# Optimization experiments

Hardware: AMD Instinct MI355X
Metric: run time of the kernel (lower is better)

Reference implementation:

```python
import jax, jax.numpy as jnp
import numpy as np

# ---- config (mirrors init_kwargs) ----
D_MODEL = 1024
D_STATE = 128
EXPAND = 2
HEADDIM = 64
D_INNER = D_MODEL * EXPAND            # 2048
NHEADS = D_INNER // HEADDIM           # 32
ROPE_FRACTION = 0.5
ROTATE_DIM = (int(D_STATE * ROPE_FRACTION) // 2) * 2   # 64
NUM_ANGLES = ROTATE_DIM // 2          # 32
A_FLOOR = 1e-4
EPS = 1e-5
IN_PROJ_DIM = 2 * D_INNER + 2 * D_STATE + 3 * NHEADS + NUM_ANGLES  # 4480
BATCH, SEQLEN = 2, 2048


def _state_rmsnorm(x, w):
    rms = jnp.sqrt(jnp.mean(x * x, axis=-1, keepdims=True) + EPS)
    return x / rms * w


def _apply_rotary_pairs(x, phase):
    # x: (b,s,h,d_state), phase: (b,s,h,num_pairs)
    if ROTATE_DIM == 0:
        return x
    x_rot = x[..., :ROTATE_DIM].reshape(*x.shape[:-1], ROTATE_DIM // 2, 2)
    x_pass = x[..., ROTATE_DIM:]
    cos = jnp.cos(phase)
    sin = jnp.sin(phase)
    real = x_rot[..., 0]
    imag = x_rot[..., 1]
    rr = real * cos - imag * sin
    ri = real * sin + imag * cos
    rotated = jnp.stack([rr, ri], axis=-1).reshape(*x.shape[:-1], ROTATE_DIM)
    if x_pass.shape[-1] == 0:
        return rotated
    return jnp.concatenate([rotated, x_pass], axis=-1)


def setup_inputs() -> dict:
    key = jax.random.key(0)
    ks = jax.random.split(key, 5)
    x = jax.random.normal(ks[0], (BATCH, SEQLEN, D_MODEL), jnp.float32)
    W_in = jax.random.normal(ks[1], (IN_PROJ_DIM, D_MODEL), jnp.float32) / np.sqrt(D_MODEL)
    # dt_bias ~ inverse-softplus of dt sampled in [dt_min, dt_max]
    dt = jnp.exp(jax.random.uniform(ks[2], (NHEADS,), jnp.float32) * (np.log(0.1) - np.log(0.001)) + np.log(0.001))
    dt = jnp.clip(dt, 1e-4)
    dt_bias = dt + jnp.log(-jnp.expm1(-dt))
    B_norm_w = jnp.ones((D_STATE,), jnp.float32)
    C_norm_w = jnp.ones((D_STATE,), jnp.float32)
    B_bias = jnp.ones((NHEADS, D_STATE), jnp.float32)
    C_bias = jnp.ones((NHEADS, D_STATE), jnp.float32)
    D_param = jnp.ones((NHEADS,), jnp.float32)
    out_norm_w = jnp.ones((D_INNER,), jnp.float32)
    W_out = jax.random.normal(ks[3], (D_MODEL, D_INNER), jnp.float32) / np.sqrt(D_INNER)
    return {"x": x, "W_in": W_in, "dt_bias": dt_bias, "B_norm_w": B_norm_w,
            "C_norm_w": C_norm_w, "B_bias": B_bias, "C_bias": C_bias,
            "D_param": D_param, "out_norm_w": out_norm_w, "W_out": W_out}


def reference(x, W_in, dt_bias, B_norm_w, C_norm_w, B_bias, C_bias, D_param, out_norm_w, W_out):
    b, s, _ = x.shape
    proj = jnp.einsum('bsd,pd->bsp', x, W_in)
    sizes = [D_INNER, D_INNER, D_STATE, D_STATE, NHEADS, NHEADS, NHEADS, NUM_ANGLES]
    offs = np.cumsum([0] + sizes)
    z, v, B_raw, C_raw, dd_dt, dd_A, trap_logits, angle_logits = [
        proj[..., offs[i]:offs[i + 1]] for i in range(8)]
    z = z.reshape(b, s, NHEADS, HEADDIM)
    v = v.reshape(b, s, NHEADS, HEADDIM)
    Bm = _state_rmsnorm(B_raw, B_norm_w)[:, :, None, :] + B_bias[None, None]   # (b,s,h,n)
    Cm = _state_rmsnorm(C_raw, C_norm_w)[:, :, None, :] + C_bias[None, None]
    dt = jax.nn.softplus(dd_dt + dt_bias[None, None])          # (b,s,h)
    A = jnp.minimum(-jax.nn.softplus(dd_A), -A_FLOOR)          # (b,s,h)
    trap = jax.nn.sigmoid(trap_logits)                          # (b,s,h)
    phase = jnp.cumsum(angle_logits, axis=1)[:, :, None, :]     # (b,s,1,angles)
    phase = jnp.broadcast_to(phase, (b, s, NHEADS, NUM_ANGLES))
    Bm = _apply_rotary_pairs(Bm, phase)
    Cm = _apply_rotary_pairs(Cm, phase)

    alpha = jnp.exp(A * dt)               # (b,s,h)
    beta = (1.0 - trap) * dt * alpha
    gamma = trap * dt

    # move time to leading for scan: (s, b, h, ...)
    def tl(a):
        return jnp.moveaxis(a, 1, 0)
    xs = (tl(alpha), tl(beta), tl(gamma), tl(Bm), tl(Cm), tl(v))

    state0 = jnp.zeros((b, NHEADS, HEADDIM, D_STATE), jnp.float32)
    pk0 = jnp.zeros((b, NHEADS, D_STATE), jnp.float32)
    pv0 = jnp.zeros((b, NHEADS, HEADDIM), jnp.float32)

    def step(carry, inp):
        state, pk, pv = carry
        a_t, b_t, g_t, k_t, q_t, v_t = inp
        prev_outer = pv[..., :, None] * pk[..., None, :]        # (b,h,p,n)
        curr_outer = v_t[..., :, None] * k_t[..., None, :]
        state = (a_t[..., None, None] * state
                 + b_t[..., None, None] * prev_outer
                 + g_t[..., None, None] * curr_outer)
        y_t = jnp.einsum('bhpn,bhn->bhp', state, q_t) + D_param[None, :, None] * v_t
        return (state, k_t, v_t), y_t

    _, ys = jax.lax.scan(step, (state0, pk0, pv0), xs)
    y = jnp.moveaxis(ys, 0, 1).reshape(b, s, D_INNER)
    z = z.reshape(b, s, D_INNER)
    # GatedRMSNorm
    rms = jnp.sqrt(jnp.mean(y * y, axis=-1, keepdims=True) + EPS)
    y = (y / rms * out_norm_w) * jax.nn.silu(z)
    return jnp.einsum('bsi,di->bsd', y, W_out)
```

## Files before the change

### kernel.cpp

```cpp
#include <hip/hip_runtime.h>
#include <math.h>

#define S_LEN 2048
#define NBATCH 2
#define DMODEL 1024
#define PDIM 4480
#define DI 2048
#define NH 32
#define HD 64
#define DS 128
#define NA 32
#define CHK 64
#define NC (S_LEN / CHK)
#define OFF_Z 0
#define OFF_V 2048
#define OFF_B 4096
#define OFF_C 4224
#define OFF_DT 4352
#define OFF_A 4384
#define OFF_TRAP 4416
#define OFF_ANG 4448

typedef __attribute__((ext_vector_type(8))) short s8v;
typedef __attribute__((ext_vector_type(4))) float f4v;

__device__ __forceinline__ float softplus_f(float x) {
    return x > 20.f ? x : log1pf(expf(x));
}

__device__ __forceinline__ ushort f2bf(float f) {
    unsigned u = __float_as_uint(f);
    unsigned r = (u + 0x7fffu + ((u >> 16) & 1u)) >> 16;
    return (ushort)r;
}

__device__ __forceinline__ uint4 pack8(const float* f) {
    uint4 o;
    o.x = (unsigned)f2bf(f[0]) | ((unsigned)f2bf(f[1]) << 16);
    o.y = (unsigned)f2bf(f[2]) | ((unsigned)f2bf(f[3]) << 16);
    o.z = (unsigned)f2bf(f[4]) | ((unsigned)f2bf(f[5]) << 16);
    o.w = (unsigned)f2bf(f[6]) | ((unsigned)f2bf(f[7]) << 16);
    return o;
}

__device__ __forceinline__ float bf2f(ushort u) {
    return __uint_as_float(((unsigned)u) << 16);
}
__device__ __forceinline__ float bf_lo(unsigned u) { return __uint_as_float(u << 16); }
__device__ __forceinline__ float bf_hi(unsigned u) { return __uint_as_float(u & 0xffff0000u); }

#define NCX  524288
#define NCWI 573440
#define NCWO 262144
__global__ __launch_bounds__(256)
void f2bf_all(const float* __restrict__ x, const float* __restrict__ wi,
              const float* __restrict__ wo, ushort* __restrict__ xbf,
              ushort* __restrict__ wibf, ushort* __restrict__ wobf) {
    int idx = blockIdx.x * 256 + threadIdx.x;
    const float* src; ushort* dst; int shift, rel;
    if (idx < NCX)              { rel = idx;               src = x;  dst = xbf;  shift = 7; }
    else if (idx < NCX + NCWI)  { rel = idx - NCX;         src = wi; dst = wibf; shift = 7; }
    else                        { rel = idx - NCX - NCWI;  src = wo; dst = wobf; shift = 8; }
    int dc = rel ^ ((rel >> shift) & 7);
    const float* ip = src + (size_t)rel * 8;
    float4 v0 = *(const float4*)ip;
    float4 v1 = *(const float4*)(ip + 4);
    uint4 o;
    o.x = (unsigned)f2bf(v0.x) | ((unsigned)f2bf(v0.y) << 16);
    o.y = (unsigned)f2bf(v0.z) | ((unsigned)f2bf(v0.w) << 16);
    o.z = (unsigned)f2bf(v1.x) | ((unsigned)f2bf(v1.y) << 16);
    o.w = (unsigned)f2bf(v1.z) | ((unsigned)f2bf(v1.w) << 16);
    *(uint4*)(dst + (size_t)dc * 8) = o;
}

__global__ __launch_bounds__(256, 4)
void gemm_bf16(const ushort* __restrict__ A, const ushort* __restrict__ B,
               float* __restrict__ C, int M, int N, int K) {
    __shared__ __align__(16) short lA[128 * 64];
    __shared__ __align__(16) short lB[128 * 64];
    int nwg = gridDim.x;
    int bid = blockIdx.x;
    int q = nwg >> 3;
    int swz = (bid & 7) * q + (bid >> 3);
    int nb = N >> 7;
    int bx = swz % nb, by = swz / nb;

    int tid = threadIdx.x;
    int wv = tid >> 6, ln = tid & 63;
    int rl = ln & 15, kg = ln >> 4, r7 = rl & 7;
    int R0 = (wv >> 1) * 64, C0 = (wv & 1) * 64;

    const ushort* Ag = A + (size_t)(by * 128 + wv * 32 + (ln >> 3)) * K + (ln & 7) * 8;
    const ushort* Bg = B + (size_t)(bx * 128 + wv * 32 + (ln >> 3)) * K + (ln & 7) * 8;
    short* lAw = lA + (wv * 32) * 64;
    short* lBw = lB + (wv * 32) * 64;

    f4v acc[4][4];
#pragma unroll
    for (int m = 0; m < 4; ++m)
#pragma unroll
        for (int n = 0; n < 4; ++n) acc[m][n] = f4v{0.f, 0.f, 0.f, 0.f};

    for (int k0 = 0; k0 < K; k0 += 64) {
        __syncthreads();
#pragma unroll
        for (int i = 0; i < 4; ++i) {
            __builtin_amdgcn_global_load_lds(
                (const __attribute__((address_space(1))) void*)(Ag + (size_t)i * 8 * K + k0),
                (__attribute__((address_space(3))) void*)(lAw + i * 8 * 64), 16, 0, 0);
            __builtin_amdgcn_global_load_lds(
                (const __attribute__((address_space(1))) void*)(Bg + (size_t)i * 8 * K + k0),
                (__attribute__((address_space(3))) void*)(lBw + i * 8 * 64), 16, 0, 0);
        }
        __syncthreads();
#pragma unroll
        for (int ks = 0; ks < 2; ++ks) {
            int kc = ks * 4 + kg;
            int co = ((kc ^ r7) << 3);
            s8v av[4], bv[4];
#pragma unroll
            for (int m = 0; m < 4; ++m)
                av[m] = *(const s8v*)&lA[(R0 + m * 16 + rl) * 64 + co];
#pragma unroll
            for (int n = 0; n < 4; ++n)
                bv[n] = *(const s8v*)&lB[(C0 + n * 16 + rl) * 64 + co];
#pragma unroll
            for (int m = 0; m < 4; ++m)
#pragma unroll
                for (int n = 0; n < 4; ++n)
                    acc[m][n] = __builtin_amdgcn_mfma_f32_16x16x32_bf16(
                        av[m], bv[n], acc[m][n], 0, 0, 0);
        }
    }
#pragma unroll
    for (int m = 0; m < 4; ++m)
#pragma unroll
        for (int n = 0; n < 4; ++n) {
            size_t row0 = (size_t)(by * 128 + R0 + m * 16 + kg * 4);
            int col = bx * 128 + C0 + n * 16 + rl;
#pragma unroll
            for (int r = 0; r < 4; ++r)
                C[(row0 + r) * N + col] = acc[m][n][r];
        }
}

__global__ __launch_bounds__(256)
void phase_kernel(const float* __restrict__ proj, float* __restrict__ cosb,
                  float* __restrict__ sinb) {
    int b = blockIdx.x >> 5;
    int j = blockIdx.x & 31;
    int tid = threadIdx.x;
    __shared__ float part[256];
    float v[8];
    float run = 0.f;
#pragma unroll
    for (int e = 0; e < 8; ++e) {
        int s = tid * 8 + e;
        v[e] = proj[((size_t)(b * S_LEN + s)) * PDIM + OFF_ANG + j];
        run += v[e];
    }
    part[tid] = run;
    __syncthreads();
    for (int off = 1; off < 256; off <<= 1) {
        float add = (tid >= off) ? part[tid - off] : 0.f;
        __syncthreads();
        part[tid] += add;
        __syncthreads();
    }
    float acc = (tid > 0) ? part[tid - 1] : 0.f;
#pragma unroll
    for (int e = 0; e < 8; ++e) {
        acc += v[e];
        int s = tid * 8 + e;
        size_t o = ((size_t)(b * S_LEN + s)) * NA + j;
        cosb[o] = cosf(acc);
        sinb[o] = sinf(acc);
    }
}

__global__ __launch_bounds__(128)
void prep_kernel(const float* __restrict__ proj, const float* __restrict__ dt_bias,
                 const float* __restrict__ Bw, const float* __restrict__ Cw,
                 const float* __restrict__ cosb, const float* __restrict__ sinb,
                 float* __restrict__ Bn, float* __restrict__ Cn,
                 float* __restrict__ ldb, float* __restrict__ wbuf,
                 float* __restrict__ pubuf) {
    size_t row = blockIdx.x;
    int b = (int)(row >> 11);
    int s = (int)(row & 2047);
    int n = threadIdx.x;
    const float* pr = proj + row * PDIM;
    float vB = pr[OFF_B + n];
    float vC = pr[OFF_C + n];
    float sB = vB * vB, sC = vC * vC;
#pragma unroll
    for (int off = 32; off >= 1; off >>= 1) {
        sB += __shfl_xor(sB, off);
        sC += __shfl_xor(sC, off);
    }
    __shared__ float redB[2], redC[2];
    if ((n & 63) == 0) { redB[n >> 6] = sB; redC[n >> 6] = sC; }
    __syncthreads();
    float rB = sqrtf((redB[0] + redB[1]) * (1.f / 128.f) + 1e-5f);
    float rC = sqrtf((redC[0] + redC[1]) * (1.f / 128.f) + 1e-5f);
    float bn = vB / rB * Bw[n];
    float cn = vC / rC * Cw[n];
    float bp = __shfl_xor(bn, 1);
    float cp = __shfl_xor(cn, 1);
    float ob = bn, oc = cn;
    if (n < 64) {
        float c = cosb[row * NA + (n >> 1)];
        float sn_ = sinb[row * NA + (n >> 1)];
        if ((n & 1) == 0) { ob = bn * c - bp * sn_; oc = cn * c - cp * sn_; }
        else              { ob = bp * sn_ + bn * c; oc = cp * sn_ + cn * c; }
    }
    Bn[row * DS + n] = ob;
    Cn[row * DS + n] = oc;
    if (n < NH) {
        int h = n;
        float dtv = softplus_f(pr[OFF_DT + h] + dt_bias[h]);
        float Av = -fmaxf(softplus_f(pr[OFF_A + h]), 1e-4f);
        float trap = 1.f / (1.f + expf(-pr[OFF_TRAP + h]));
        size_t o = ((size_t)(b * NH + h)) * S_LEN + s;
        ldb[o]   = Av * dtv;
        wbuf[o]  = trap * dtv;
        pubuf[o] = (1.f - trap) * dtv;
    }
}

__global__ __launch_bounds__(256)
void lcum_kernel(float* __restrict__ ell) {
    size_t row = blockIdx.x;
    int tid = threadIdx.x;
    float* p = ell + row * S_LEN;
    float v[8];
    float run = 0.f;
#pragma unroll
    for (int e = 0; e < 8; ++e) { v[e] = p[tid * 8 + e]; run += v[e]; }
    __shared__ float part[256];
    part[tid] = run;
    __syncthreads();
    for (int off = 1; off < 256; off <<= 1) {
        float add = (tid >= off) ? part[tid - off] : 0.f;
        __syncthreads();
        part[tid] += add;
        __syncthreads();
    }
    float acc = (tid > 0) ? part[tid - 1] : 0.f;
#pragma unroll
    for (int e = 0; e < 8; ++e) { acc += v[e]; p[tid * 8 + e] = acc; }
}

__device__ __forceinline__ void build32v(
    float* vals, const float* __restrict__ br, const float* __restrict__ bias,
    const float* __restrict__ cr, const float* __restrict__ sr, int rot) {
    float bv[32], bi[32];
#pragma unroll
    for (int j = 0; j < 8; ++j) *(float4*)&bv[j * 4] = *(const float4*)(br + j * 4);
#pragma unroll
    for (int j = 0; j < 8; ++j) *(float4*)&bi[j * 4] = *(const float4*)(bias + j * 4);
    if (rot) {
        float cf[16], sf[16];
#pragma unroll
        for (int j = 0; j < 4; ++j) {
            *(float4*)&cf[j * 4] = *(const float4*)(cr + j * 4);
            *(float4*)&sf[j * 4] = *(const float4*)(sr + j * 4);
        }
#pragma unroll
        for (int a = 0; a < 16; ++a) {
            float c = cf[a], s = sf[a], e = bi[2 * a], o = bi[2 * a + 1];
            vals[2 * a]     = bv[2 * a]     + e * c - o * s;
            vals[2 * a + 1] = bv[2 * a + 1] + e * s + o * c;
        }
    } else {
#pragma unroll
        for (int j = 0; j < 32; ++j) vals[j] = bv[j] + bi[j];
    }
}

__global__ __launch_bounds__(256, 4)
void delta_kernel(const float* __restrict__ proj, const float* __restrict__ Bn,
                  const float* __restrict__ cosb, const float* __restrict__ sinb,
                  const float* __restrict__ ell, const float* __restrict__ wbuf,
                  const float* __restrict__ pubuf, const float* __restrict__ B_bias,
                  ushort* __restrict__ dstate, ushort* __restrict__ vtbuf,
                  float* __restrict__ rbuf) {
    __shared__ __align__(16) ushort KT[DS * CHK];
    __shared__ __align__(16) ushort cVT[HD * CHK];
    __shared__ __align__(16) ushort VT[HD * CHK];
    int blk = blockIdx.x;
    int c = blk & (NC - 1);
    int h = (blk >> 5) & (NH - 1);
    int b = blk >> 10;
    int tid = threadIdx.x;
    size_t row0 = (size_t)b * S_LEN + c * CHK;
    size_t bh = (size_t)b * NH + h;
    int i = tid >> 2, q4 = tid & 3;

    size_t so = bh * S_LEN + c * CHK + i;
    float llast = ell[bh * S_LEN + c * CHK + CHK - 1];
    float li = ell[so];
    float u = wbuf[so];
    if (c * CHK + i < S_LEN - 1) u += pubuf[so + 1];
    float coef = expf(llast - li) * u;
    if (tid == 0) {
        float base = (c == 0) ? 0.f : ell[bh * S_LEN + c * CHK - 1];
        rbuf[blk] = expf(llast - base);
    }
    {
        int n0 = q4 * 32;
        float vals[32];
        build32v(vals, Bn + (row0 + i) * DS + n0, B_bias + h * DS + n0,
                 cosb + (row0 + i) * NA + q4 * 16, sinb + (row0 + i) * NA + q4 * 16,
                 q4 < 2);
#pragma unroll
        for (int j = 0; j < 32; ++j) {
            int n = n0 + j;
            KT[n * 64 + (((i >> 3) ^ (n & 7)) << 3) + (i & 7)] = f2bf(vals[j]);
        }
    }
    {
        int p0 = q4 * 16;
        float vr[16];
        const float* vp = proj + (row0 + i) * PDIM + OFF_V + h * HD + p0;
#pragma unroll
        for (int j = 0; j < 4; ++j) *(float4*)&vr[j * 4] = *(const float4*)(vp + j * 4);
#pragma unroll
        for (int j = 0; j < 16; ++j) {
            int p = p0 + j;
            int addr = p * 64 + (((i >> 3) ^ (p & 7)) << 3) + (i & 7);
            VT[addr]  = f2bf(vr[j]);
            cVT[addr] = f2bf(vr[j] * coef);
        }
    }
    __syncthreads();
    {
        const uint4* vs = (const uint4*)VT;
        uint4* vd = (uint4*)(vtbuf + (size_t)blk * (HD * CHK));
        vd[tid] = vs[tid];
        vd[tid + 256] = vs[tid + 256];
    }
    int wv = tid >> 6, ln = tid & 63, rl = ln & 15, kg = ln >> 4;
    int pA = wv * 16 + rl;
    s8v aV[2];
#pragma unroll
    for (int ks = 0; ks < 2; ++ks)
        aV[ks] = *(const s8v*)&cVT[pA * 64 + (((ks * 4 + kg) ^ (pA & 7)) << 3)];
    ushort* dp = dstate + (size_t)blk * (HD * DS);
#pragma unroll
    for (int nt = 0; nt < 8; ++nt) {
        int nB = nt * 16 + rl;
        f4v dacc = f4v{0.f, 0.f, 0.f, 0.f};
#pragma unroll
        for (int ks = 0; ks < 2; ++ks) {
            s8v bK = *(const s8v*)&KT[nB * 64 + (((ks * 4 + kg) ^ (nB & 7)) << 3)];
            dacc = __builtin_amdgcn_mfma_f32_16x16x32_bf16(aV[ks], bK, dacc, 0, 0, 0);
        }
#pragma unroll
        for (int r = 0; r < 4; ++r) {
            int p = wv * 16 + kg * 4 + r;
            int n = nt * 16 + rl;
            dp[p * DS + (((n >> 3) ^ (p & 7)) << 3) + (n & 7)] = f2bf(dacc[r]);
        }
    }
}

__global__ __launch_bounds__(256)
void state_prop(ushort* __restrict__ dstate, const float* __restrict__ rbuf) {
    size_t bh = blockIdx.x;
    int tid = threadIdx.x;
    float st[32];
#pragma unroll
    for (int j = 0; j < 32; ++j) st[j] = 0.f;
    uint4* base = (uint4*)dstate;
    size_t b0 = bh * NC * 1024ull;
    uint4 nxt[4];
#pragma unroll
    for (int j = 0; j < 4; ++j) nxt[j] = base[b0 + tid * 4 + j];
    for (int c = 0; c < NC; ++c) {
        uint4 cur[4];
#pragma unroll
        for (int j = 0; j < 4; ++j) cur[j] = nxt[j];
        if (c + 1 < NC) {
#pragma unroll
            for (int j = 0; j < 4; ++j)
                nxt[j] = base[b0 + (size_t)(c + 1) * 1024 + tid * 4 + j];
        }
        float r = rbuf[bh * NC + c];
        uint4 outv[4];
#pragma unroll
        for (int j = 0; j < 4; ++j) {
            unsigned uu[4] = {cur[j].x, cur[j].y, cur[j].z, cur[j].w};
            unsigned oo[4];
#pragma unroll
            for (int e = 0; e < 4; ++e) {
                float d0 = bf_lo(uu[e]), d1 = bf_hi(uu[e]);
                int ix = j * 8 + e * 2;
                oo[e] = (unsigned)f2bf(st[ix]) | ((unsigned)f2bf(st[ix + 1]) << 16);
                st[ix]     = fmaf(r, st[ix], d0);
                st[ix + 1] = fmaf(r, st[ix + 1], d1);
            }
            outv[j] = uint4{oo[0], oo[1], oo[2], oo[3]};
        }
#pragma unroll
        for (int j = 0; j < 4; ++j)
            base[b0 + (size_t)c * 1024 + tid * 4 + j] = outv[j];
    }
}

__global__ __launch_bounds__(256, 3)
void out_kernel(const float* __restrict__ Bn, const float* __restrict__ Cn,
                const float* __restrict__ cosb, const float* __restrict__ sinb,
                const float* __restrict__ ell, const float* __restrict__ wbuf,
                const float* __restrict__ pubuf, const float* __restrict__ B_bias,
                const float* __restrict__ C_bias, const ushort* __restrict__ dstate,
                const ushort* __restrict__ vtbuf, float* __restrict__ yb) {
    __shared__ __align__(16) ushort Qb[CHK * DS];
    __shared__ __align__(16) ushort Kb[CHK * DS];
    __shared__ __align__(16) ushort VTb[HD * CHK];
    __shared__ __align__(16) ushort PTb[CHK * CHK];
    __shared__ float s_et[CHK], s_fs[CHK], s_w[CHK];
    int blk = blockIdx.x;
    int c = blk & (NC - 1);
    int h = (blk >> 5) & (NH - 1);
    int b = blk >> 10;
    int tid = threadIdx.x;
    size_t row0 = (size_t)b * S_LEN + c * CHK;
    size_t bh = (size_t)b * NH + h;
    int i = tid >> 2, q4 = tid & 3;
    int wv2 = tid >> 6, ln = tid & 63;

    {
        const ushort* vg = vtbuf + (size_t)blk * (HD * CHK);
#pragma unroll
        for (int k = 0; k < 2; ++k) {
            int ch = wv2 * 128 + k * 64;
            __builtin_amdgcn_global_load_lds(
                (const __attribute__((address_space(1))) void*)(vg + (size_t)(ch + ln) * 8),
                (__attribute__((address_space(3))) void*)(VTb + ch * 8), 16, 0, 0);
        }
    }
    if (q4 == 0) {
        size_t so = bh * S_LEN + c * CHK + i;
        float base = (c == 0) ? 0.f : ell[bh * S_LEN + c * CHK - 1];
        float lp = ell[so] - base;
        float wv_ = wbuf[so];
        float u = wv_;
        if (c * CHK + i < S_LEN - 1) u += pubuf[so + 1];
        s_et[i] = expf(lp);
        s_fs[i] = u * expf(fminf(-lp, 80.f));
        s_w[i] = wv_;
    }
    {
        int n0 = q4 * 32;
        float vals[32];
        build32v(vals, Cn + (row0 + i) * DS + n0, C_bias + h * DS + n0,
                 cosb + (row0 + i) * NA + q4 * 16, sinb + (row0 + i) * NA + q4 * 16,
                 q4 < 2);
#pragma unroll
        for (int j = 0; j < 4; ++j) {
            int cc = (q4 * 4 + j) ^ (i & 7);
            *(uint4*)&Qb[i * 128 + cc * 8] = pack8(&vals[j * 8]);
        }
    }
    {
        int n0 = q4 * 32;
        float vals[32];
        build32v(vals, Bn + (row0 + i) * DS + n0, B_bias + h * DS + n0,
                 cosb + (row0 + i) * NA + q4 * 16, sinb + (row0 + i) * NA + q4 * 16,
                 q4 < 2);
#pragma unroll
        for (int j = 0; j < 4; ++j) {
            int cc = (q4 * 4 + j) ^ (i & 7);
            *(uint4*)&Kb[i * 128 + cc * 8] = pack8(&vals[j * 8]);
        }
    }
    __syncthreads();

    int rl = ln & 15, kg = ln >> 4;
    int tA = wv2 * 16 + rl;
    s8v aQ[4];
#pragma unroll
    for (int kc = 0; kc < 4; ++kc)
        aQ[kc] = *(const s8v*)&Qb[tA * 128 + (((kc * 4 + kg) ^ (tA & 7)) << 3)];
    f4v pacc[4];
#pragma unroll
    for (int st = 0; st < 4; ++st) pacc[st] = f4v{0.f, 0.f, 0.f, 0.f};
#pragma unroll
    for (int st = 0; st < 4; ++st) {
        int sB = st * 16 + rl;
#pragma unroll
        for (int kc = 0; kc < 4; ++kc) {
            s8v bK = *(const s8v*)&Kb[sB * 128 + (((kc * 4 + kg) ^ (sB & 7)) << 3)];
            pacc[st] = __builtin_amdgcn_mfma_f32_16x16x32_bf16(aQ[kc], bK, pacc[st], 0, 0, 0);
        }
    }
    __syncthreads();

    {
        const ushort* sg = dstate + (size_t)blk * (CHK * DS);
#pragma unroll
        for (int k = 0; k < 4; ++k) {
            int ch = wv2 * 256 + k * 64;
            __builtin_amdgcn_global_load_lds(
                (const __attribute__((address_space(1))) void*)(sg + (size_t)(ch + ln) * 8),
                (__attribute__((address_space(3))) void*)(Kb + ch * 8), 16, 0, 0);
        }
    }
#pragma unroll
    for (int st = 0; st < 4; ++st) {
        int s = st * 16 + rl;
#pragma unroll
        for (int r = 0; r < 4; ++r) {
            int t2 = wv2 * 16 + kg * 4 + r;
            float m;
            if (s < t2)       m = s_et[t2] * s_fs[s];
            else if (s == t2) m = s_w[t2];
            else              m = 0.f;
            PTb[t2 * 64 + (((s >> 3) ^ (t2 & 7)) << 3) + (s & 7)] = f2bf(pacc[st][r] * m);
        }
    }
    __syncthreads();

    s8v aP[2];
#pragma unroll
    for (int ks = 0; ks < 2; ++ks)
        aP[ks] = *(const s8v*)&PTb[tA * 64 + (((ks * 4 + kg) ^ (tA & 7)) << 3)];
    f4v y1[4], y2[4];
#pragma unroll
    for (int pt = 0; pt < 4; ++pt) { y1[pt] = f4v{0.f,0.f,0.f,0.f}; y2[pt] = f4v{0.f,0.f,0.f,0.f}; }
#pragma unroll
    for (int pt = 0; pt < 4; ++pt) {
        int pB = pt * 16 + rl;
#pragma unroll
        for (int ks = 0; ks < 2; ++ks) {
            s8v bV = *(const s8v*)&VTb[pB * 64 + (((ks * 4 + kg) ^ (pB & 7)) << 3)];
            y1[pt] = __builtin_amdgcn_mfma_f32_16x16x32_bf16(aP[ks], bV, y1[pt], 0, 0, 0);
        }
#pragma unroll
        for (int kc = 0; kc < 4; ++kc) {
            s8v bS = *(const s8v*)&Kb[pB * 128 + (((kc * 4 + kg) ^ (pB & 7)) << 3)];
            y2[pt] = __builtin_amdgcn_mfma_f32_16x16x32_bf16(aQ[kc], bS, y2[pt], 0, 0, 0);
        }
    }
    float* yp = yb + (size_t)blk * (CHK * HD);
#pragma unroll
    for (int pt = 0; pt < 4; ++pt) {
#pragma unroll
        for (int r = 0; r < 4; ++r) {
            int t2 = wv2 * 16 + kg * 4 + r;
            int p = pt * 16 + rl;
            yp[t2 * HD + p] = y1[pt][r] + s_et[t2] * y2[pt][r];
        }
    }
}

__global__ __launch_bounds__(256)
void ynorm_kernel(const float* __restrict__ yb, const float* __restrict__ proj,
                  const float* __restrict__ w, const float* __restrict__ D_param,
                  ushort* __restrict__ ybf) {
    size_t row = blockIdx.x;
    int b = (int)(row >> 11);
    int s = (int)(row & 2047);
    int c = s >> 6, t = s & 63;
    int tid = threadIdx.x;
    int hh = tid >> 3;
    int p0 = (tid * 8) & 63;
    const float* yr = yb + (((size_t)(b * NH + hh) * NC + c) * CHK + t) * HD + p0;
    float4 v0 = *(const float4*)yr;
    float4 v1 = *(const float4*)(yr + 4);
    const float* vr = proj + row * (size_t)PDIM + OFF_V + tid * 8;
    float4 vv0 = *(const float4*)vr;
    float4 vv1 = *(const float4*)(vr + 4);
    float Dp = D_param[hh];
    float yv[8] = {v0.x + Dp * vv0.x, v0.y + Dp * vv0.y, v0.z + Dp * vv0.z, v0.w + Dp * vv0.w,
                   v1.x + Dp * vv1.x, v1.y + Dp * vv1.y, v1.z + Dp * vv1.z, v1.w + Dp * vv1.w};
    float ss = 0.f;
#pragma unroll
    for (int e = 0; e < 8; ++e) ss += yv[e] * yv[e];
#pragma unroll
    for (int off = 32; off >= 1; off >>= 1) ss += __shfl_xor(ss, off);
    __shared__ float red[4];
    if ((tid & 63) == 0) red[tid >> 6] = ss;
    __syncthreads();
    float tot = red[0] + red[1] + red[2] + red[3];
    float rinv = 1.f / sqrtf(tot * (1.f / 2048.f) + 1e-5f);
    const float* zr = proj + row * (size_t)PDIM + OFF_Z;
    float4 z0 = *(const float4*)(zr + tid * 8);
    float4 z1 = *(const float4*)(zr + tid * 8 + 4);
    float4 w0 = *(const float4*)(w + tid * 8);
    float4 w1 = *(const float4*)(w + tid * 8 + 4);
    float zv[8] = {z0.x, z0.y, z0.z, z0.w, z1.x, z1.y, z1.z, z1.w};
    float wv[8] = {w0.x, w0.y, w0.z, w0.w, w1.x, w1.y, w1.z, w1.w};
    ushort u[8];
#pragma unroll
    for (int e = 0; e < 8; ++e) {
        float sil = zv[e] / (1.f + expf(-zv[e]));
        u[e] = f2bf(yv[e] * rinv * wv[e] * sil);
    }
    int dstc = (tid & ~7) | ((tid & 7) ^ ((int)row & 7));
    uint4 o;
    o.x = (unsigned)u[0] | ((unsigned)u[1] << 16);
    o.y = (unsigned)u[2] | ((unsigned)u[3] << 16);
    o.z = (unsigned)u[4] | ((unsigned)u[5] << 16);
    o.w = (unsigned)u[6] | ((unsigned)u[7] << 16);
    *(uint4*)(ybf + row * (size_t)DI + dstc * 8) = o;
}

extern "C" void kernel_launch(void* const* d_in, const int* in_sizes, int n_in,
                              void* d_out, int out_size, void* d_ws, size_t ws_size,
                              hipStream_t stream) {
    const float* x          = (const float*)d_in[0];
    const float* W_in       = (const float*)d_in[1];
    const float* dt_bias    = (const float*)d_in[2];
    const float* B_norm_w   = (const float*)d_in[3];
    const float* C_norm_w   = (const float*)d_in[4];
    const float* B_bias     = (const float*)d_in[5];
    const float* C_bias     = (const float*)d_in[6];
    const float* D_param    = (const float*)d_in[7];
    const float* out_norm_w = (const float*)d_in[8];
    const float* W_out      = (const float*)d_in[9];
    float* out = (float*)d_out;

    const size_t M = (size_t)NBATCH * S_LEN;
    const size_t NBLK = (size_t)NBATCH * NH * NC;
    float* ws = (float*)d_ws;
    size_t off = 0;
    float* proj  = ws + off; off += M * PDIM;
    float* cosb  = ws + off; off += M * NA;
    float* sinb  = ws + off; off += M * NA;
    float* Bn    = ws + off; off += M * DS;
    float* Cn    = ws + off; off += M * DS;
    float* ell   = ws + off; off += (size_t)NBATCH * NH * S_LEN;
    float* wbuf  = ws + off; off += (size_t)NBATCH * NH * S_LEN;
    float* pubuf = ws + off; off += (size_t)NBATCH * NH * S_LEN;
    float* yb    = ws + off; off += NBLK * CHK * HD;
    float* rbuf  = ws + off; off += NBLK;
    ushort* xbf  = (ushort*)(ws + off); off += M * DMODEL / 2;
    ushort* wibf = (ushort*)(ws + off); off += (size_t)PDIM * DMODEL / 2;
    ushort* wobf = (ushort*)(ws + off); off += (size_t)DMODEL * DI / 2;
    ushort* ybf  = (ushort*)(ws + off); off += M * DI / 2;
    ushort* dstate = (ushort*)(ws + off); off += NBLK * CHK * DS / 2;
    ushort* vtbuf  = (ushort*)(ws + off); off += NBLK * HD * CHK / 2;

    f2bf_all<<<dim3((NCX + NCWI + NCWO) / 256), 256, 0, stream>>>(
        x, W_in, W_out, xbf, wibf, wobf);
    gemm_bf16<<<dim3((PDIM / 128) * (int)(M / 128)), 256, 0, stream>>>(xbf, wibf, proj, (int)M, PDIM, DMODEL);
    phase_kernel<<<dim3(NBATCH * NA), 256, 0, stream>>>(proj, cosb, sinb);
    prep_kernel<<<dim3((int)M), 128, 0, stream>>>(proj, dt_bias, B_norm_w, C_norm_w,
                                                  cosb, sinb, Bn, Cn, ell, wbuf, pubuf);
    lcum_kernel<<<dim3(NBATCH * NH), 256, 0, stream>>>(ell);
    delta_kernel<<<dim3((int)NBLK), 256, 0, stream>>>(proj, Bn, cosb, sinb, ell,
                                                      wbuf, pubuf, B_bias, dstate,
                                                      vtbuf, rbuf);
    state_prop<<<dim3(NBATCH * NH), 256, 0, stream>>>(dstate, rbuf);
    out_kernel<<<dim3((int)NBLK), 256, 0, stream>>>(Bn, Cn, cosb, sinb, ell,
                                                    wbuf, pubuf, B_bias, C_bias,
                                                    dstate, vtbuf, yb);
    ynorm_kernel<<<dim3((int)M), 256, 0, stream>>>(yb, proj, out_norm_w, D_param, ybf);
    gemm_bf16<<<dim3((DMODEL / 128) * (int)(M / 128)), 256, 0, stream>>>(ybf, wobf, out, (int)M, DMODEL, DI);
}
```

Before: 256.6 us.

## Cache rotated K in delta kernel, stream to out kernel, shrink its LDS

The delta kernel now writes the rotated, biased B (K) chunk as bf16 to a new global buffer. The out kernel loads it asynchronously into LDS instead of rebuilding it from Bn, cosb and sinb. The out kernel also drops its separate P tile and per-row shared arrays: it reuses the Q buffer for P and computes decay factors in registers, cutting LDS so it can target 4 blocks per SM. The GEMM launch bound drops from 4 to 2 blocks, trading occupancy for more registers. This adds global write and read traffic for the K buffer.

```diff
diff --git a/kernel.cpp b/kernel.cpp
--- a/kernel.cpp
+++ b/kernel.cpp
@@ -73,7 +73,7 @@
     *(uint4*)(dst + (size_t)dc * 8) = o;
 }
 
-__global__ __launch_bounds__(256, 4)
+__global__ __launch_bounds__(256, 2)
 void gemm_bf16(const ushort* __restrict__ A, const ushort* __restrict__ B,
                float* __restrict__ C, int M, int N, int K) {
     __shared__ __align__(16) short lA[128 * 64];
@@ -284,7 +284,7 @@
                   const float* __restrict__ ell, const float* __restrict__ wbuf,
                   const float* __restrict__ pubuf, const float* __restrict__ B_bias,
                   ushort* __restrict__ dstate, ushort* __restrict__ vtbuf,
-                  float* __restrict__ rbuf) {
+                  ushort* __restrict__ kbuf, float* __restrict__ rbuf) {
     __shared__ __align__(16) ushort KT[DS * CHK];
     __shared__ __align__(16) ushort cVT[HD * CHK];
     __shared__ __align__(16) ushort VT[HD * CHK];
@@ -318,6 +318,12 @@
             int n = n0 + j;
             KT[n * 64 + (((i >> 3) ^ (n & 7)) << 3) + (i & 7)] = f2bf(vals[j]);
         }
+        ushort* kd = kbuf + (size_t)blk * (CHK * DS);
+#pragma unroll
+        for (int j = 0; j < 4; ++j) {
+            int cc = (q4 * 4 + j) ^ (i & 7);
+            *(uint4*)&kd[i * 128 + cc * 8] = pack8(&vals[j * 8]);
+        }
     }
     {
         int p0 = q4 * 16;
@@ -408,18 +414,16 @@
     }
 }
 
-__global__ __launch_bounds__(256, 3)
-void out_kernel(const float* __restrict__ Bn, const float* __restrict__ Cn,
-                const float* __restrict__ cosb, const float* __restrict__ sinb,
-                const float* __restrict__ ell, const float* __restrict__ wbuf,
-                const float* __restrict__ pubuf, const float* __restrict__ B_bias,
+__global__ __launch_bounds__(256, 4)
+void out_kernel(const float* __restrict__ Cn, const float* __restrict__ cosb,
+                const float* __restrict__ sinb, const float* __restrict__ ell,
+                const float* __restrict__ wbuf, const float* __restrict__ pubuf,
                 const float* __restrict__ C_bias, const ushort* __restrict__ dstate,
-                const ushort* __restrict__ vtbuf, float* __restrict__ yb) {
+                const ushort* __restrict__ vtbuf, const ushort* __restrict__ kbuf,
+                float* __restrict__ yb) {
     __shared__ __align__(16) ushort Qb[CHK * DS];
     __shared__ __align__(16) ushort Kb[CHK * DS];
     __shared__ __align__(16) ushort VTb[HD * CHK];
-    __shared__ __align__(16) ushort PTb[CHK * CHK];
-    __shared__ float s_et[CHK], s_fs[CHK], s_w[CHK];
     int blk = blockIdx.x;
     int c = blk & (NC - 1);
     int h = (blk >> 5) & (NH - 1);
@@ -431,6 +435,14 @@
     int wv2 = tid >> 6, ln = tid & 63;
 
     {
+        const ushort* kg_ = kbuf + (size_t)blk * (CHK * DS);
+#pragma unroll
+        for (int k = 0; k < 4; ++k) {
+            int ch = wv2 * 256 + k * 64;
+            __builtin_amdgcn_global_load_lds(
+                (const __attribute__((address_space(1))) void*)(kg_ + (size_t)(ch + ln) * 8),
+                (__attribute__((address_space(3))) void*)(Kb + ch * 8), 16, 0, 0);
+        }
         const ushort* vg = vtbuf + (size_t)blk * (HD * CHK);
 #pragma unroll
         for (int k = 0; k < 2; ++k) {
@@ -439,17 +451,6 @@
                 (const __attribute__((address_space(1))) void*)(vg + (size_t)(ch + ln) * 8),
                 (__attribute__((address_space(3))) void*)(VTb + ch * 8), 16, 0, 0);
         }
-    }
-    if (q4 == 0) {
-        size_t so = bh * S_LEN + c * CHK + i;
-        float base = (c == 0) ? 0.f : ell[bh * S_LEN + c * CHK - 1];
-        float lp = ell[so] - base;
-        float wv_ = wbuf[so];
-        float u = wv_;
-        if (c * CHK + i < S_LEN - 1) u += pubuf[so + 1];
-        s_et[i] = expf(lp);
-        s_fs[i] = u * expf(fminf(-lp, 80.f));
-        s_w[i] = wv_;
     }
     {
         int n0 = q4 * 32;
@@ -463,18 +464,6 @@
             *(uint4*)&Qb[i * 128 + cc * 8] = pack8(&vals[j * 8]);
         }
     }
-    {
-        int n0 = q4 * 32;
-        float vals[32];
-        build32v(vals, Bn + (row0 + i) * DS + n0, B_bias + h * DS + n0,
-                 cosb + (row0 + i) * NA + q4 * 16, sinb + (row0 + i) * NA + q4 * 16,
-                 q4 < 2);
-#pragma unroll
-        for (int j = 0; j < 4; ++j) {
-            int cc = (q4 * 4 + j) ^ (i & 7);
-            *(uint4*)&Kb[i * 128 + cc * 8] = pack8(&vals[j * 8]);
-        }
-    }
     __syncthreads();
 
     int rl = ln & 15, kg = ln >> 4;
@@ -507,15 +496,35 @@
                 (__attribute__((address_space(3))) void*)(Kb + ch * 8), 16, 0, 0);
         }
     }
+    size_t so0 = bh * S_LEN + c * CHK;
+    float basev = (c == 0) ? 0.f : ell[so0 - 1];
+    int t2r0 = wv2 * 16 + kg * 4;
+    float et[4], wr[4];
+#pragma unroll
+    for (int r = 0; r < 4; ++r) {
+        size_t so = so0 + t2r0 + r;
+        et[r] = expf(ell[so] - basev);
+        wr[r] = wbuf[so];
+    }
+    float fs[4];
 #pragma unroll
     for (int st = 0; st < 4; ++st) {
         int s = st * 16 + rl;
+        size_t sos = so0 + s;
+        float u = wbuf[sos];
+        if (c * CHK + s < S_LEN - 1) u += pubuf[sos + 1];
+        fs[st] = u * expf(fminf(basev - ell[sos], 80.f));
+    }
+    ushort* PTb = Qb;
+#pragma unroll
+    for (int st = 0; st < 4; ++st) {
+        int s = st * 16 + rl;
 #pragma unroll
         for (int r = 0; r < 4; ++r) {
-            int t2 = wv2 * 16 + kg * 4 + r;
+            int t2 = t2r0 + r;
             float m;
-            if (s < t2)       m = s_et[t2] * s_fs[s];
-            else if (s == t2) m = s_w[t2];
+            if (s < t2)       m = et[r] * fs[st];
+            else if (s == t2) m = wr[r];
             else              m = 0.f;
             PTb[t2 * 64 + (((s >> 3) ^ (t2 & 7)) << 3) + (s & 7)] = f2bf(pacc[st][r] * m);
         }
@@ -548,9 +557,9 @@
     for (int pt = 0; pt < 4; ++pt) {
 #pragma unroll
         for (int r = 0; r < 4; ++r) {
-            int t2 = wv2 * 16 + kg * 4 + r;
+            int t2 = t2r0 + r;
             int p = pt * 16 + rl;
-            yp[t2 * HD + p] = y1[pt][r] + s_et[t2] * y2[pt][r];
+            yp[t2 * HD + p] = y1[pt][r] + et[r] * y2[pt][r];
         }
     }
 }
@@ -642,6 +651,7 @@
     ushort* ybf  = (ushort*)(ws + off); off += M * DI / 2;
     ushort* dstate = (ushort*)(ws + off); off += NBLK * CHK * DS / 2;
     ushort* vtbuf  = (ushort*)(ws + off); off += NBLK * HD * CHK / 2;
+    ushort* kbuf   = (ushort*)(ws + off); off += NBLK * CHK * DS / 2;
 
     f2bf_all<<<dim3((NCX + NCWI + NCWO) / 256), 256, 0, stream>>>(
         x, W_in, W_out, xbf, wibf, wobf);
@@ -652,11 +662,11 @@
     lcum_kernel<<<dim3(NBATCH * NH), 256, 0, stream>>>(ell);
     delta_kernel<<<dim3((int)NBLK), 256, 0, stream>>>(proj, Bn, cosb, sinb, ell,
                                                       wbuf, pubuf, B_bias, dstate,
-                                                      vtbuf, rbuf);
+                                                      vtbuf, kbuf, rbuf);
     state_prop<<<dim3(NBATCH * NH), 256, 0, stream>>>(dstate, rbuf);
-    out_kernel<<<dim3((int)NBLK), 256, 0, stream>>>(Bn, Cn, cosb, sinb, ell,
-                                                    wbuf, pubuf, B_bias, C_bias,
-                                                    dstate, vtbuf, yb);
+    out_kernel<<<dim3((int)NBLK), 256, 0, stream>>>(Cn, cosb, sinb, ell,
+                                                    wbuf, pubuf, C_bias,
+                                                    dstate, vtbuf, kbuf, yb);
     ynorm_kernel<<<dim3((int)M), 256, 0, stream>>>(yb, proj, out_norm_w, D_param, ybf);
     gemm_bf16<<<dim3((DMODEL / 128) * (int)(M / 128)), 256, 0, stream>>>(ybf, wobf, out, (int)M, DMODEL, DI);
 }
```

Measured after the change: 252.6 us. About the same (-1.5%).
